# Kernel optimization log

Measured on AMD Instinct MI355X. Metric: run time of the kernel, lower is better.

The kernel has to match this reference:

```python
import jax, jax.numpy as jnp
import numpy as np
from jax import lax

D_MODEL = 1024
EXPAND = 2
D_INNER = EXPAND * D_MODEL  # 2048
D_STATE = 16
D_CONV = 4
DT_RANK = -(-D_INNER // 16)  # ceil(d_inner/16) = 128
BATCH, SEQLEN = 2, 1024
LN_EPS = 1e-5


def setup_inputs() -> dict:
    key = jax.random.key(0)
    ks = jax.random.split(key, 8)
    s = lambda n: 1.0 / np.sqrt(n)
    x = jax.random.normal(ks[0], (BATCH, SEQLEN, D_MODEL), jnp.float32)
    ln_gamma = jnp.ones((D_MODEL,), jnp.float32)
    ln_beta = jnp.zeros((D_MODEL,), jnp.float32)
    in_proj_w = jax.random.normal(ks[1], (D_MODEL, 2 * D_INNER), jnp.float32) * s(D_MODEL)
    conv_w = jax.random.normal(ks[2], (D_INNER, D_CONV), jnp.float32) * s(D_CONV)
    conv_b = jnp.zeros((D_INNER,), jnp.float32)
    x_proj_w = jax.random.normal(ks[3], (D_INNER, DT_RANK + 2 * D_STATE), jnp.float32) * s(D_INNER)
    dt_proj_w = jax.random.uniform(ks[4], (DT_RANK, D_INNER), jnp.float32,
                                   -DT_RANK ** -0.5, DT_RANK ** -0.5)
    # dt bias init: inverse-softplus of dt ~ LogUniform(1e-3, 1e-1)
    dt = jnp.exp(jax.random.uniform(ks[5], (D_INNER,), jnp.float32)
                 * (np.log(0.1) - np.log(0.001)) + np.log(0.001))
    dt = jnp.clip(dt, 1e-4)
    dt_proj_b = dt + jnp.log(-jnp.expm1(-dt))
    A_log = jnp.log(jnp.tile(jnp.arange(1, D_STATE + 1, dtype=jnp.float32)[None, :],
                             (D_INNER, 1)))  # (D_INNER, D_STATE)
    D_param = jnp.ones((D_INNER,), jnp.float32)
    out_proj_w = jax.random.normal(ks[6], (D_INNER, D_MODEL), jnp.float32) * s(D_INNER)
    return {"x": x, "ln_gamma": ln_gamma, "ln_beta": ln_beta, "in_proj_w": in_proj_w,
            "conv_w": conv_w, "conv_b": conv_b, "x_proj_w": x_proj_w,
            "dt_proj_w": dt_proj_w, "dt_proj_b": dt_proj_b, "A_log": A_log,
            "D_param": D_param, "out_proj_w": out_proj_w}


def _layernorm(x, gamma, beta):
    mu = jnp.mean(x, -1, keepdims=True)
    var = jnp.mean(jnp.square(x - mu), -1, keepdims=True)
    return (x - mu) * lax.rsqrt(var + LN_EPS) * gamma + beta


def reference(x, ln_gamma, ln_beta, in_proj_w, conv_w, conv_b, x_proj_w,
              dt_proj_w, dt_proj_b, A_log, D_param, out_proj_w):
    B, L, _ = x.shape
    residual = x
    h = _layernorm(x, ln_gamma, ln_beta)
    xz = h @ in_proj_w                               # (B, L, 2*Di)
    xb, z = jnp.split(xz, 2, axis=-1)                # each (B, L, Di)

    # Depthwise causal conv1d (left pad d_conv-1, truncate to L)
    xp = jnp.pad(xb, ((0, 0), (D_CONV - 1, 0), (0, 0)))
    xc = sum(xp[:, k:k + L, :] * conv_w[:, k] for k in range(D_CONV)) + conv_b
    xb = jax.nn.silu(xc)                             # (B, L, Di)

    # Selective SSM
    xpj = xb @ x_proj_w                              # (B, L, dt_rank + 2N)
    dt_r = xpj[..., :DT_RANK]
    B_mat = xpj[..., DT_RANK:DT_RANK + D_STATE]      # (B, L, N)
    C_mat = xpj[..., DT_RANK + D_STATE:]             # (B, L, N)
    delta = jax.nn.softplus(dt_r @ dt_proj_w + dt_proj_b)  # (B, L, Di)
    A = -jnp.exp(A_log)                              # (Di, N)
    dA = jnp.exp(delta[..., None] * A)               # (B, L, Di, N)
    dBx = delta[..., None] * B_mat[:, :, None, :] * xb[..., None]  # (B, L, Di, N)

    def step(hcar, inp):
        dA_t, dBx_t, C_t = inp                       # (B,Di,N),(B,Di,N),(B,N)
        hcar = dA_t * hcar + dBx_t
        y_t = jnp.einsum('bdn,bn->bd', hcar, C_t)
        return hcar, y_t

    h0 = jnp.zeros((B, D_INNER, D_STATE), xb.dtype)
    _, ys = lax.scan(step, h0, (dA.transpose(1, 0, 2, 3),
                                dBx.transpose(1, 0, 2, 3),
                                C_mat.transpose(1, 0, 2)))
    y = ys.transpose(1, 0, 2) + xb * D_param         # (B, L, Di)

    y = y * jax.nn.silu(z)
    return y @ out_proj_w + residual
```

## Files before the change

kernel.cpp:

```cpp
#include <hip/hip_runtime.h>
#include <hip/hip_bf16.h>

#define D_MODEL 1024
#define D_INNER 2048
#define NPROJ   4096
#define D_STATE 16
#define DT_RANK 128
#define XPJ_N   160
#define SEQLEN  1024
#define BATCH   2
#define NTOK    2048
#define CHUNK   32
#define NCHUNK  (SEQLEN / CHUNK)
#define LOG2_NCHUNK 5
#define SPLITK  8
#define OP_SPLITK 4

typedef short short8 __attribute__((ext_vector_type(8)));
typedef float f32x4 __attribute__((ext_vector_type(4)));

__device__ __forceinline__ float sigmoidf_(float x) { return 1.f / (1.f + __expf(-x)); }
__device__ __forceinline__ ushort f2bf_bits(float f) {
    __hip_bfloat16 h = __float2bfloat16(f);
    return *(ushort*)&h;
}
__device__ __forceinline__ float bf2f(ushort u) {
    union { unsigned int i; float f; } v;
    v.i = ((unsigned int)u) << 16;
    return v.f;
}
__device__ __forceinline__ float quad_xor1_add(float p) {
    int q = __builtin_amdgcn_mov_dpp(__float_as_int(p), 0xB1, 0xF, 0xF, true);
    return p + __int_as_float(q);
}
__device__ __forceinline__ float quad_xor2_add(float p) {
    int q = __builtin_amdgcn_mov_dpp(__float_as_int(p), 0x4E, 0xF, 0xF, true);
    return p + __int_as_float(q);
}

__global__ __launch_bounds__(256) void ln_kernel(const float* __restrict__ x,
                                                 const float* __restrict__ g,
                                                 const float* __restrict__ be,
                                                 ushort* __restrict__ hb)
{
    int row = blockIdx.x;
    const float4* xr = (const float4*)(x + (long)row * D_MODEL);
    float4 v = xr[threadIdx.x];
    float s1 = v.x + v.y + v.z + v.w;
    float s2 = v.x*v.x + v.y*v.y + v.z*v.z + v.w*v.w;
    for (int off = 32; off >= 1; off >>= 1) {
        s1 += __shfl_down(s1, off);
        s2 += __shfl_down(s2, off);
    }
    __shared__ float red[8];
    int wid = threadIdx.x >> 6;
    if ((threadIdx.x & 63) == 0) { red[wid] = s1; red[4 + wid] = s2; }
    __syncthreads();
    float mu  = (red[0] + red[1] + red[2] + red[3]) * (1.f / D_MODEL);
    float ex2 = (red[4] + red[5] + red[6] + red[7]) * (1.f / D_MODEL);
    float inv = rsqrtf(ex2 - mu * mu + 1e-5f);
    float4 g4 = ((const float4*)g)[threadIdx.x];
    float4 b4 = ((const float4*)be)[threadIdx.x];
    ushort4 o;
    o.x = f2bf_bits((v.x - mu) * inv * g4.x + b4.x);
    o.y = f2bf_bits((v.y - mu) * inv * g4.y + b4.y);
    o.z = f2bf_bits((v.z - mu) * inv * g4.z + b4.z);
    o.w = f2bf_bits((v.w - mu) * inv * g4.w + b4.w);
    *(ushort4*)(hb + (long)row * D_MODEL + threadIdx.x * 4) = o;
}

__global__ __launch_bounds__(256) void transpose_bf16_kernel(const float* __restrict__ in,
                                                             ushort* __restrict__ out,
                                                             int R, int C)
{
    __shared__ float tile[64][65];
    int c0 = blockIdx.x * 64, r0 = blockIdx.y * 64;
    #pragma unroll
    for (int i = 0; i < 16; ++i) {
        int idx = threadIdx.x + i * 256;
        int r = idx >> 6, c = idx & 63;
        tile[r][c] = (r0 + r < R && c0 + c < C) ? in[(long)(r0 + r) * C + (c0 + c)] : 0.f;
    }
    __syncthreads();
    #pragma unroll
    for (int i = 0; i < 16; ++i) {
        int idx = threadIdx.x + i * 256;
        int cc = idx >> 6, rr = idx & 63;
        if (c0 + cc < C && r0 + rr < R)
            out[(long)(c0 + cc) * R + (r0 + rr)] = f2bf_bits(tile[rr][cc]);
    }
}

template <int EPI, int OBF>
__global__ __launch_bounds__(256) void gemm_mfma_kernel(const ushort* __restrict__ A,
                                                        const ushort* __restrict__ Bt,
                                                        const float* __restrict__ bias,
                                                        float* __restrict__ Cf,
                                                        ushort* __restrict__ Cb,
                                                        int M, int N, int K, int lda, int ldb)
{
    long zoff = (long)blockIdx.z;
    A  += zoff * K;
    Bt += zoff * K;
    if (OBF == 0) Cf += zoff * (long)M * N;
    __shared__ __align__(16) ushort Al[128 * 32];
    __shared__ __align__(16) ushort Bl[128 * 32];
    int tid = threadIdx.x;
    int lane = tid & 63;
    int w = tid >> 6, wr = w >> 1, wc = w & 1;
    int m0 = blockIdx.y * 128, n0 = blockIdx.x * 128;
    f32x4 acc[4][4];
    #pragma unroll
    for (int m = 0; m < 4; ++m)
        #pragma unroll
        for (int n = 0; n < 4; ++n) acc[m][n] = (f32x4){0.f, 0.f, 0.f, 0.f};
    int l15 = lane & 15, kq = lane >> 4;

    for (int k0 = 0; k0 < K; k0 += 32) {
        #pragma unroll
        for (int i = 0; i < 2; ++i) {
            int s = i * 256 + tid;
            int row = s >> 2, kg = s & 3;
            int kgl = kg ^ ((row >> 1) & 3);
            __builtin_amdgcn_global_load_lds(
                (const __attribute__((address_space(1))) void*)(A + (long)(m0 + row) * lda + k0 + kgl * 8),
                (__attribute__((address_space(3))) void*)(Al + s * 8), 16, 0, 0);
            __builtin_amdgcn_global_load_lds(
                (const __attribute__((address_space(1))) void*)(Bt + (long)(n0 + row) * ldb + k0 + kgl * 8),
                (__attribute__((address_space(3))) void*)(Bl + s * 8), 16, 0, 0);
        }
        __syncthreads();
        short8 af[4], bf[4];
        #pragma unroll
        for (int m = 0; m < 4; ++m) {
            int row = wr * 64 + m * 16 + l15;
            af[m] = *(const short8*)&Al[row * 32 + (kq ^ ((row >> 1) & 3)) * 8];
        }
        #pragma unroll
        for (int n = 0; n < 4; ++n) {
            int row = wc * 64 + n * 16 + l15;
            bf[n] = *(const short8*)&Bl[row * 32 + (kq ^ ((row >> 1) & 3)) * 8];
        }
        #pragma unroll
        for (int m = 0; m < 4; ++m)
            #pragma unroll
            for (int n = 0; n < 4; ++n)
                acc[m][n] = __builtin_amdgcn_mfma_f32_16x16x32_bf16(af[m], bf[n], acc[m][n], 0, 0, 0);
        __syncthreads();
    }
    #pragma unroll
    for (int m = 0; m < 4; ++m) {
        #pragma unroll
        for (int n = 0; n < 4; ++n) {
            #pragma unroll
            for (int r = 0; r < 4; ++r) {
                int row = m0 + wr * 64 + m * 16 + kq * 4 + r;
                int col = n0 + wc * 64 + n * 16 + l15;
                float v = acc[m][n][r];
                if (EPI == 1) {
                    v += bias[col];
                    v = (v > 20.f) ? v : log1pf(__expf(v));
                }
                if (OBF) Cb[(long)row * N + col] = f2bf_bits(v);
                else     Cf[(long)row * N + col] = v;
            }
        }
    }
}

template <int EPI, int OBF>
__global__ __launch_bounds__(256) void gemm_mfma64_kernel(const ushort* __restrict__ A,
                                                          const ushort* __restrict__ Bt,
                                                          const float* __restrict__ bias,
                                                          float* __restrict__ Cf,
                                                          ushort* __restrict__ Cb,
                                                          int M, int N, int K)
{
    __shared__ __align__(16) ushort Al[128 * 32];
    __shared__ __align__(16) ushort Bl[64 * 32];
    int tid = threadIdx.x;
    int lane = tid & 63;
    int w = tid >> 6, wr = w >> 1, wc = w & 1;
    int m0 = blockIdx.y * 128, n0 = blockIdx.x * 64;
    f32x4 acc[4][2];
    #pragma unroll
    for (int m = 0; m < 4; ++m)
        #pragma unroll
        for (int n = 0; n < 2; ++n) acc[m][n] = (f32x4){0.f, 0.f, 0.f, 0.f};
    int l15 = lane & 15, kq = lane >> 4;

    for (int k0 = 0; k0 < K; k0 += 32) {
        #pragma unroll
        for (int i = 0; i < 2; ++i) {
            int s = i * 256 + tid;
            int row = s >> 2, kg = s & 3;
            int kgl = kg ^ ((row >> 1) & 3);
            __builtin_amdgcn_global_load_lds(
                (const __attribute__((address_space(1))) void*)(A + (long)(m0 + row) * K + k0 + kgl * 8),
                (__attribute__((address_space(3))) void*)(Al + s * 8), 16, 0, 0);
        }
        {
            int s = tid;
            int row = s >> 2, kg = s & 3;
            int kgl = kg ^ ((row >> 1) & 3);
            __builtin_amdgcn_global_load_lds(
                (const __attribute__((address_space(1))) void*)(Bt + (long)(n0 + row) * K + k0 + kgl * 8),
                (__attribute__((address_space(3))) void*)(Bl + s * 8), 16, 0, 0);
        }
        __syncthreads();
        short8 af[4], bf[2];
        #pragma unroll
        for (int m = 0; m < 4; ++m) {
            int row = wr * 64 + m * 16 + l15;
            af[m] = *(const short8*)&Al[row * 32 + (kq ^ ((row >> 1) & 3)) * 8];
        }
        #pragma unroll
        for (int n = 0; n < 2; ++n) {
            int row = wc * 32 + n * 16 + l15;
            bf[n] = *(const short8*)&Bl[row * 32 + (kq ^ ((row >> 1) & 3)) * 8];
        }
        #pragma unroll
        for (int m = 0; m < 4; ++m)
            #pragma unroll
            for (int n = 0; n < 2; ++n)
                acc[m][n] = __builtin_amdgcn_mfma_f32_16x16x32_bf16(af[m], bf[n], acc[m][n], 0, 0, 0);
        __syncthreads();
    }
    #pragma unroll
    for (int m = 0; m < 4; ++m) {
        #pragma unroll
        for (int n = 0; n < 2; ++n) {
            #pragma unroll
            for (int r = 0; r < 4; ++r) {
                int row = m0 + wr * 64 + m * 16 + kq * 4 + r;
                int col = n0 + wc * 32 + n * 16 + l15;
                float v = acc[m][n][r];
                if (EPI == 1) {
                    v += bias[col];
                    v = (v > 20.f) ? v : log1pf(__expf(v));
                }
                if (OBF) Cb[(long)row * N + col] = f2bf_bits(v);
                else     Cf[(long)row * N + col] = v;
            }
        }
    }
}

__global__ __launch_bounds__(256) void reduce_out_kernel(const float* __restrict__ Ppart,
                                                         const float* __restrict__ resid,
                                                         float* __restrict__ out)
{
    long i = (long)blockIdx.x * 256 + threadIdx.x;
    const long STRIDE = (long)NTOK * D_MODEL / 4;
    float4 s = ((const float4*)Ppart)[i];
    #pragma unroll
    for (int k = 1; k < OP_SPLITK; ++k) {
        float4 p = ((const float4*)Ppart)[k * STRIDE + i];
        s.x += p.x; s.y += p.y; s.z += p.z; s.w += p.w;
    }
    float4 r = ((const float4*)resid)[i];
    s.x += r.x; s.y += r.y; s.z += r.z; s.w += r.w;
    ((float4*)out)[i] = s;
}

__global__ __launch_bounds__(256) void gemm4_mfma_kernel(const ushort* __restrict__ A,
                                                         const ushort* __restrict__ Bt,
                                                         float* __restrict__ Ppart,
                                                         int M, int K)
{
    __shared__ __align__(16) ushort Al[64 * 32];
    __shared__ __align__(16) ushort Bl[160 * 32];
    int tid = threadIdx.x;
    int lane = tid & 63;
    int w = tid >> 6, wr = w >> 1, wc = w & 1;
    int sk = blockIdx.x;
    int m0 = blockIdx.y * 64;
    int kbase = sk * (K / SPLITK);
    f32x4 acc[2][5];
    #pragma unroll
    for (int m = 0; m < 2; ++m)
        #pragma unroll
        for (int n = 0; n < 5; ++n) acc[m][n] = (f32x4){0.f, 0.f, 0.f, 0.f};
    int l15 = lane & 15, kq = lane >> 4;

    for (int ks = 0; ks < K / SPLITK; ks += 32) {
        int k0 = kbase + ks;
        {
            int s = tid;
            int row = s >> 2, kg = s & 3;
            int kgl = kg ^ ((row >> 1) & 3);
            __builtin_amdgcn_global_load_lds(
                (const __attribute__((address_space(1))) void*)(A + (long)(m0 + row) * K + k0 + kgl * 8),
                (__attribute__((address_space(3))) void*)(Al + s * 8), 16, 0, 0);
        }
        #pragma unroll
        for (int i = 0; i < 3; ++i) {
            int s = i * 256 + tid;
            if (s < 640) {
                int row = s >> 2, kg = s & 3;
                int kgl = kg ^ ((row >> 1) & 3);
                __builtin_amdgcn_global_load_lds(
                    (const __attribute__((address_space(1))) void*)(Bt + (long)row * K + k0 + kgl * 8),
                    (__attribute__((address_space(3))) void*)(Bl + s * 8), 16, 0, 0);
            }
        }
        __syncthreads();
        short8 af[2], bf[5];
        #pragma unroll
        for (int m = 0; m < 2; ++m) {
            int row = wr * 32 + m * 16 + l15;
            af[m] = *(const short8*)&Al[row * 32 + (kq ^ ((row >> 1) & 3)) * 8];
        }
        #pragma unroll
        for (int n = 0; n < 5; ++n) {
            int row = wc * 80 + n * 16 + l15;
            bf[n] = *(const short8*)&Bl[row * 32 + (kq ^ ((row >> 1) & 3)) * 8];
        }
        #pragma unroll
        for (int m = 0; m < 2; ++m)
            #pragma unroll
            for (int n = 0; n < 5; ++n)
                acc[m][n] = __builtin_amdgcn_mfma_f32_16x16x32_bf16(af[m], bf[n], acc[m][n], 0, 0, 0);
        __syncthreads();
    }
    float* P = Ppart + (long)sk * M * XPJ_N;
    #pragma unroll
    for (int m = 0; m < 2; ++m) {
        #pragma unroll
        for (int n = 0; n < 5; ++n) {
            #pragma unroll
            for (int r = 0; r < 4; ++r) {
                int row = m0 + wr * 32 + m * 16 + kq * 4 + r;
                int col = wc * 80 + n * 16 + l15;
                P[(long)row * XPJ_N + col] = acc[m][n][r];
            }
        }
    }
}

__global__ __launch_bounds__(256) void reduce_xpj_kernel(const float* __restrict__ Ppart,
                                                         float* __restrict__ xpj,
                                                         ushort* __restrict__ dtr)
{
    long i = (long)blockIdx.x * 256 + threadIdx.x;
    float s = 0.f;
    #pragma unroll
    for (int k = 0; k < SPLITK; ++k) s += Ppart[k * (long)NTOK * XPJ_N + i];
    xpj[i] = s;
    int col = (int)(i % XPJ_N);
    long row = i / XPJ_N;
    if (col < DT_RANK) dtr[row * DT_RANK + col] = f2bf_bits(s);
}

__global__ __launch_bounds__(256) void conv_silu_kernel(const ushort* __restrict__ xzb,
                                                        const float* __restrict__ cw,
                                                        const float* __restrict__ cb,
                                                        ushort* __restrict__ xbb)
{
    long i = (long)blockIdx.x * 256 + threadIdx.x;
    int d = (int)(i & (D_INNER - 1));
    long tok = i >> 11;
    int l = (int)(tok & (SEQLEN - 1));
    float w0 = cw[d * 4 + 0], w1 = cw[d * 4 + 1], w2 = cw[d * 4 + 2], w3 = cw[d * 4 + 3];
    float acc = cb[d];
    acc += bf2f(xzb[tok * NPROJ + d]) * w3;
    if (l >= 1) acc += bf2f(xzb[(tok - 1) * NPROJ + d]) * w2;
    if (l >= 2) acc += bf2f(xzb[(tok - 2) * NPROJ + d]) * w1;
    if (l >= 3) acc += bf2f(xzb[(tok - 3) * NPROJ + d]) * w0;
    float v = acc * sigmoidf_(acc);
    xbb[i] = f2bf_bits(v);
}

__global__ __launch_bounds__(256) void scan_partial_kernel(const ushort* __restrict__ deltab,
                                                           const ushort* __restrict__ xbb,
                                                           const float* __restrict__ xpj,
                                                           const float* __restrict__ A_log,
                                                           float* __restrict__ Pout,
                                                           float* __restrict__ Hout)
{
    int tid = threadIdx.x;
    int j = tid & 3, grp = tid >> 2;
    long gidx = (long)blockIdx.x * 64 + grp;
    int d = (int)(gidx & (D_INNER - 1));
    int c = (int)((gidx >> 11) & (NCHUNK - 1));
    int b = (int)(gidx >> (11 + LOG2_NCHUNK));
    float4 al = *(const float4*)&A_log[d * D_STATE + 4 * j];
    float a0 = -__expf(al.x), a1 = -__expf(al.y), a2 = -__expf(al.z), a3 = -__expf(al.w);
    float h0 = 0.f, h1 = 0.f, h2 = 0.f, h3 = 0.f, cum = 0.f;
    long tok0 = (long)b * SEQLEN + c * CHUNK;
    const ushort* dp = deltab + tok0 * D_INNER + d;
    const ushort* xp = xbb + tok0 * D_INNER + d;
    const float* Bp = xpj + tok0 * XPJ_N + DT_RANK + 4 * j;
    for (int t = 0; t < CHUNK; ++t) {
        float dl = bf2f(*dp);
        float x  = bf2f(*xp);
        float4 Bv = *(const float4*)Bp;
        dp += D_INNER; xp += D_INNER; Bp += XPJ_N;
        cum += dl;
        float ux = dl * x;
        h0 = __expf(dl * a0) * h0 + ux * Bv.x;
        h1 = __expf(dl * a1) * h1 + ux * Bv.y;
        h2 = __expf(dl * a2) * h2 + ux * Bv.z;
        h3 = __expf(dl * a3) * h3 + ux * Bv.w;
    }
    long o = gidx * D_STATE + 4 * j;
    *(float4*)&Pout[o] = (float4){__expf(a0 * cum), __expf(a1 * cum), __expf(a2 * cum), __expf(a3 * cum)};
    *(float4*)&Hout[o] = (float4){h0, h1, h2, h3};
}

__global__ __launch_bounds__(256) void scan_chunkscan_kernel(const float* __restrict__ P,
                                                             const float* __restrict__ H,
                                                             float* __restrict__ hinit)
{
    long i = (long)blockIdx.x * 256 + threadIdx.x;
    int n = (int)(i & (D_STATE - 1));
    int d = (int)((i >> 4) & (D_INNER - 1));
    int b = (int)(i >> 15);
    float h = 0.f;
    for (int c = 0; c < NCHUNK; ++c) {
        long o = ((((long)b * NCHUNK + c) * D_INNER + d) * D_STATE) + n;
        hinit[o] = h;
        h = P[o] * h + H[o];
    }
}

__global__ __launch_bounds__(256) void scan_final_kernel(const ushort* __restrict__ deltab,
                                                         const ushort* __restrict__ xbb,
                                                         const float* __restrict__ xpj,
                                                         const ushort* __restrict__ xzb,
                                                         const float* __restrict__ A_log,
                                                         const float* __restrict__ Dp,
                                                         const float* __restrict__ hinit,
                                                         ushort* __restrict__ yb)
{
    int tid = threadIdx.x;
    int j = tid & 3, grp = tid >> 2;
    long gidx = (long)blockIdx.x * 64 + grp;
    int d = (int)(gidx & (D_INNER - 1));
    int c = (int)((gidx >> 11) & (NCHUNK - 1));
    int b = (int)(gidx >> (11 + LOG2_NCHUNK));
    float4 al = *(const float4*)&A_log[d * D_STATE + 4 * j];
    float a0 = -__expf(al.x), a1 = -__expf(al.y), a2 = -__expf(al.z), a3 = -__expf(al.w);
    float dpar = Dp[d];
    float4 hv = *(const float4*)&hinit[gidx * D_STATE + 4 * j];
    float h0 = hv.x, h1 = hv.y, h2 = hv.z, h3 = hv.w;
    long tok0 = (long)b * SEQLEN + c * CHUNK;
    const ushort* dp = deltab + tok0 * D_INNER + d;
    const ushort* xp = xbb + tok0 * D_INNER + d;
    const float* Bp = xpj + tok0 * XPJ_N + DT_RANK + 4 * j;
    const float* Cp = Bp + D_STATE;
    const ushort* zp = xzb + tok0 * NPROJ + D_INNER + d;
    ushort* yp = yb + tok0 * D_INNER + d;
    for (int t = 0; t < CHUNK; ++t) {
        float dl = bf2f(*dp);
        float x  = bf2f(*xp);
        float4 Bv = *(const float4*)Bp;
        float4 Cv = *(const float4*)Cp;
        dp += D_INNER; xp += D_INNER; Bp += XPJ_N; Cp += XPJ_N;
        float ux = dl * x;
        h0 = __expf(dl * a0) * h0 + ux * Bv.x;
        h1 = __expf(dl * a1) * h1 + ux * Bv.y;
        h2 = __expf(dl * a2) * h2 + ux * Bv.z;
        h3 = __expf(dl * a3) * h3 + ux * Bv.w;
        float p = h0 * Cv.x + h1 * Cv.y + h2 * Cv.z + h3 * Cv.w;
        p = quad_xor1_add(p);
        p = quad_xor2_add(p);
        if (j == 0) {
            float z = bf2f(*zp);
            float y = p + x * dpar;
            *yp = f2bf_bits(y * (z * sigmoidf_(z)));
        }
        zp += NPROJ; yp += D_INNER;
    }
}

extern "C" void kernel_launch(void* const* d_in, const int* in_sizes, int n_in,
                              void* d_out, int out_size, void* d_ws, size_t ws_size,
                              hipStream_t stream) {
    const float* x         = (const float*)d_in[0];
    const float* ln_gamma  = (const float*)d_in[1];
    const float* ln_beta   = (const float*)d_in[2];
    const float* in_proj_w = (const float*)d_in[3];
    const float* conv_w    = (const float*)d_in[4];
    const float* conv_b    = (const float*)d_in[5];
    const float* x_proj_w  = (const float*)d_in[6];
    const float* dt_proj_w = (const float*)d_in[7];
    const float* dt_proj_b = (const float*)d_in[8];
    const float* A_log     = (const float*)d_in[9];
    const float* D_param   = (const float*)d_in[10];
    const float* out_proj_w= (const float*)d_in[11];
    float* out = (float*)d_out;

    float* p = (float*)d_ws;
    ushort* hb      = (ushort*)p; p += 1048576;
    ushort* W2T     = (ushort*)p; p += 2097152;
    ushort* W7T     = (ushort*)p; p += 1048576;
    ushort* XPT     = (ushort*)p; p += 163840;
    ushort* DTT     = (ushort*)p; p += 131072;
    ushort* xz_bf16 = (ushort*)p; p += 4194304;
    ushort* xb_bf16 = (ushort*)p; p += 2097152;
    float*  xpj     = p;          p += 327680;
    ushort* dtr     = (ushort*)p; p += 131072;
    ushort* delta_bf16 = (ushort*)p; p += 2097152;
    float*  Ppart   = p;          p += 2621440;
    float*  Pbuf    = p;          p += 2097152;
    float*  Hbuf    = p;          p += 2097152;
    float*  hinit   = p;          p += 2097152;
    ushort* y_bf16  = (ushort*)p; p += 2097152;
    float*  PpartO  = p;          p += 8388608;

    transpose_bf16_kernel<<<dim3(NPROJ / 64, D_MODEL / 64), 256, 0, stream>>>(
        in_proj_w, W2T, D_MODEL, NPROJ);
    transpose_bf16_kernel<<<dim3(D_MODEL / 64, D_INNER / 64), 256, 0, stream>>>(
        out_proj_w, W7T, D_INNER, D_MODEL);
    transpose_bf16_kernel<<<dim3((XPJ_N + 63) / 64, D_INNER / 64), 256, 0, stream>>>(
        x_proj_w, XPT, D_INNER, XPJ_N);
    transpose_bf16_kernel<<<dim3(D_INNER / 64, DT_RANK / 64), 256, 0, stream>>>(
        dt_proj_w, DTT, DT_RANK, D_INNER);

    ln_kernel<<<NTOK, 256, 0, stream>>>(x, ln_gamma, ln_beta, hb);

    gemm_mfma_kernel<0, 1><<<dim3(NPROJ / 128, NTOK / 128), 256, 0, stream>>>(
        hb, W2T, nullptr, nullptr, xz_bf16, NTOK, NPROJ, D_MODEL, D_MODEL, D_MODEL);

    conv_silu_kernel<<<(NTOK * D_INNER) / 256, 256, 0, stream>>>(
        xz_bf16, conv_w, conv_b, xb_bf16);

    gemm4_mfma_kernel<<<dim3(SPLITK, NTOK / 64), 256, 0, stream>>>(
        xb_bf16, XPT, Ppart, NTOK, D_INNER);
    reduce_xpj_kernel<<<(NTOK * XPJ_N) / 256, 256, 0, stream>>>(Ppart, xpj, dtr);

    gemm_mfma64_kernel<1, 1><<<dim3(D_INNER / 64, NTOK / 128), 256, 0, stream>>>(
        dtr, DTT, dt_proj_b, nullptr, delta_bf16, NTOK, D_INNER, DT_RANK);

    scan_partial_kernel<<<(BATCH * NCHUNK * D_INNER) / 64, 256, 0, stream>>>(
        delta_bf16, xb_bf16, xpj, A_log, Pbuf, Hbuf);
    scan_chunkscan_kernel<<<(BATCH * D_INNER * D_STATE) / 256, 256, 0, stream>>>(
        Pbuf, Hbuf, hinit);
    scan_final_kernel<<<(BATCH * NCHUNK * D_INNER) / 64, 256, 0, stream>>>(
        delta_bf16, xb_bf16, xpj, xz_bf16, A_log, D_param, hinit, y_bf16);

    gemm_mfma_kernel<0, 0><<<dim3(D_MODEL / 128, NTOK / 128, OP_SPLITK), 256, 0, stream>>>(
        y_bf16, W7T, nullptr, PpartO, nullptr, NTOK, D_MODEL, D_INNER / OP_SPLITK,
        D_INNER, D_INNER);
    reduce_out_kernel<<<(NTOK * D_MODEL / 4) / 256, 256, 0, stream>>>(PpartO, x, out);
}
```

Before: 203.4 us.

## Map one thread per channel with all 16 states in the scan kernels

Both chunked-scan kernels now give each thread one inner channel holding all 16 state values in registers, instead of spreading the states over four lanes. This removes the DPP cross-lane reduction, the single-lane output write and the replicated delta/x/z loads per quad, and makes the bf16 loads coalesced across channels. The exp calls switch to exp2f with A prescaled by log2(e). In exchange the grid drops from 2048 to 512 blocks, so each thread carries more registers and there is less parallelism to hide latency.

```diff
diff --git a/kernel.cpp b/kernel.cpp
--- a/kernel.cpp
+++ b/kernel.cpp
@@ -29,14 +29,7 @@
     v.i = ((unsigned int)u) << 16;
     return v.f;
 }
-__device__ __forceinline__ float quad_xor1_add(float p) {
-    int q = __builtin_amdgcn_mov_dpp(__float_as_int(p), 0xB1, 0xF, 0xF, true);
-    return p + __int_as_float(q);
-}
-__device__ __forceinline__ float quad_xor2_add(float p) {
-    int q = __builtin_amdgcn_mov_dpp(__float_as_int(p), 0x4E, 0xF, 0xF, true);
-    return p + __int_as_float(q);
-}
+#define LOG2E 1.44269504088896f
 
 __global__ __launch_bounds__(256) void ln_kernel(const float* __restrict__ x,
                                                  const float* __restrict__ g,
@@ -371,6 +364,7 @@
     xbb[i] = f2bf_bits(v);
 }
 
+
 __global__ __launch_bounds__(256) void scan_partial_kernel(const ushort* __restrict__ deltab,
                                                            const ushort* __restrict__ xbb,
                                                            const float* __restrict__ xpj,
@@ -378,34 +372,51 @@
                                                            float* __restrict__ Pout,
                                                            float* __restrict__ Hout)
 {
-    int tid = threadIdx.x;
-    int j = tid & 3, grp = tid >> 2;
-    long gidx = (long)blockIdx.x * 64 + grp;
-    int d = (int)(gidx & (D_INNER - 1));
-    int c = (int)((gidx >> 11) & (NCHUNK - 1));
-    int b = (int)(gidx >> (11 + LOG2_NCHUNK));
-    float4 al = *(const float4*)&A_log[d * D_STATE + 4 * j];
-    float a0 = -__expf(al.x), a1 = -__expf(al.y), a2 = -__expf(al.z), a3 = -__expf(al.w);
-    float h0 = 0.f, h1 = 0.f, h2 = 0.f, h3 = 0.f, cum = 0.f;
+    int blk = blockIdx.x;
+    int db = blk & 7;
+    int c  = (blk >> 3) & (NCHUNK - 1);
+    int b  = blk >> (3 + LOG2_NCHUNK);
+    int d  = db * 256 + threadIdx.x;
+    float a[16], h[16];
+    #pragma unroll
+    for (int q = 0; q < 4; ++q) {
+        float4 al = *(const float4*)&A_log[d * D_STATE + q * 4];
+        a[q*4+0] = -__expf(al.x) * LOG2E;
+        a[q*4+1] = -__expf(al.y) * LOG2E;
+        a[q*4+2] = -__expf(al.z) * LOG2E;
+        a[q*4+3] = -__expf(al.w) * LOG2E;
+    }
+    #pragma unroll
+    for (int n = 0; n < 16; ++n) h[n] = 0.f;
+    float cum = 0.f;
     long tok0 = (long)b * SEQLEN + c * CHUNK;
     const ushort* dp = deltab + tok0 * D_INNER + d;
     const ushort* xp = xbb + tok0 * D_INNER + d;
-    const float* Bp = xpj + tok0 * XPJ_N + DT_RANK + 4 * j;
+    const float* Bbase = xpj + tok0 * XPJ_N + DT_RANK;
     for (int t = 0; t < CHUNK; ++t) {
-        float dl = bf2f(*dp);
-        float x  = bf2f(*xp);
-        float4 Bv = *(const float4*)Bp;
-        dp += D_INNER; xp += D_INNER; Bp += XPJ_N;
+        float dl = bf2f(dp[(long)t * D_INNER]);
+        float x  = bf2f(xp[(long)t * D_INNER]);
+        float ux = dl * x;
         cum += dl;
-        float ux = dl * x;
-        h0 = __expf(dl * a0) * h0 + ux * Bv.x;
-        h1 = __expf(dl * a1) * h1 + ux * Bv.y;
-        h2 = __expf(dl * a2) * h2 + ux * Bv.z;
-        h3 = __expf(dl * a3) * h3 + ux * Bv.w;
-    }
-    long o = gidx * D_STATE + 4 * j;
-    *(float4*)&Pout[o] = (float4){__expf(a0 * cum), __expf(a1 * cum), __expf(a2 * cum), __expf(a3 * cum)};
-    *(float4*)&Hout[o] = (float4){h0, h1, h2, h3};
+        const float* Bp = Bbase + (long)t * XPJ_N;
+        #pragma unroll
+        for (int q = 0; q < 4; ++q) {
+            float4 Bv = *(const float4*)(Bp + q * 4);
+            h[q*4+0] = exp2f(dl * a[q*4+0]) * h[q*4+0] + ux * Bv.x;
+            h[q*4+1] = exp2f(dl * a[q*4+1]) * h[q*4+1] + ux * Bv.y;
+            h[q*4+2] = exp2f(dl * a[q*4+2]) * h[q*4+2] + ux * Bv.z;
+            h[q*4+3] = exp2f(dl * a[q*4+3]) * h[q*4+3] + ux * Bv.w;
+        }
+    }
+    long chbase = ((long)(b * NCHUNK + c) * D_INNER + d) * D_STATE;
+    #pragma unroll
+    for (int q = 0; q < 4; ++q) {
+        float4 pv = {exp2f(a[q*4+0] * cum), exp2f(a[q*4+1] * cum),
+                     exp2f(a[q*4+2] * cum), exp2f(a[q*4+3] * cum)};
+        *(float4*)&Pout[chbase + q * 4] = pv;
+        float4 hv = {h[q*4+0], h[q*4+1], h[q*4+2], h[q*4+3]};
+        *(float4*)&Hout[chbase + q * 4] = hv;
+    }
 }
 
 __global__ __launch_bounds__(256) void scan_chunkscan_kernel(const float* __restrict__ P,
@@ -433,44 +444,52 @@
                                                          const float* __restrict__ hinit,
                                                          ushort* __restrict__ yb)
 {
-    int tid = threadIdx.x;
-    int j = tid & 3, grp = tid >> 2;
-    long gidx = (long)blockIdx.x * 64 + grp;
-    int d = (int)(gidx & (D_INNER - 1));
-    int c = (int)((gidx >> 11) & (NCHUNK - 1));
-    int b = (int)(gidx >> (11 + LOG2_NCHUNK));
-    float4 al = *(const float4*)&A_log[d * D_STATE + 4 * j];
-    float a0 = -__expf(al.x), a1 = -__expf(al.y), a2 = -__expf(al.z), a3 = -__expf(al.w);
+    int blk = blockIdx.x;
+    int db = blk & 7;
+    int c  = (blk >> 3) & (NCHUNK - 1);
+    int b  = blk >> (3 + LOG2_NCHUNK);
+    int d  = db * 256 + threadIdx.x;
+    float a[16], h[16];
+    #pragma unroll
+    for (int q = 0; q < 4; ++q) {
+        float4 al = *(const float4*)&A_log[d * D_STATE + q * 4];
+        a[q*4+0] = -__expf(al.x) * LOG2E;
+        a[q*4+1] = -__expf(al.y) * LOG2E;
+        a[q*4+2] = -__expf(al.z) * LOG2E;
+        a[q*4+3] = -__expf(al.w) * LOG2E;
+    }
+    long chbase = ((long)(b * NCHUNK + c) * D_INNER + d) * D_STATE;
+    #pragma unroll
+    for (int q = 0; q < 4; ++q) {
+        float4 hv = *(const float4*)&hinit[chbase + q * 4];
+        h[q*4+0] = hv.x; h[q*4+1] = hv.y; h[q*4+2] = hv.z; h[q*4+3] = hv.w;
+    }
     float dpar = Dp[d];
-    float4 hv = *(const float4*)&hinit[gidx * D_STATE + 4 * j];
-    float h0 = hv.x, h1 = hv.y, h2 = hv.z, h3 = hv.w;
     long tok0 = (long)b * SEQLEN + c * CHUNK;
     const ushort* dp = deltab + tok0 * D_INNER + d;
     const ushort* xp = xbb + tok0 * D_INNER + d;
-    const float* Bp = xpj + tok0 * XPJ_N + DT_RANK + 4 * j;
-    const float* Cp = Bp + D_STATE;
     const ushort* zp = xzb + tok0 * NPROJ + D_INNER + d;
     ushort* yp = yb + tok0 * D_INNER + d;
+    const float* Bbase = xpj + tok0 * XPJ_N + DT_RANK;
     for (int t = 0; t < CHUNK; ++t) {
-        float dl = bf2f(*dp);
-        float x  = bf2f(*xp);
-        float4 Bv = *(const float4*)Bp;
-        float4 Cv = *(const float4*)Cp;
-        dp += D_INNER; xp += D_INNER; Bp += XPJ_N; Cp += XPJ_N;
+        float dl = bf2f(dp[(long)t * D_INNER]);
+        float x  = bf2f(xp[(long)t * D_INNER]);
+        float z  = bf2f(zp[(long)t * NPROJ]);
         float ux = dl * x;
-        h0 = __expf(dl * a0) * h0 + ux * Bv.x;
-        h1 = __expf(dl * a1) * h1 + ux * Bv.y;
-        h2 = __expf(dl * a2) * h2 + ux * Bv.z;
-        h3 = __expf(dl * a3) * h3 + ux * Bv.w;
-        float p = h0 * Cv.x + h1 * Cv.y + h2 * Cv.z + h3 * Cv.w;
-        p = quad_xor1_add(p);
-        p = quad_xor2_add(p);
-        if (j == 0) {
-            float z = bf2f(*zp);
-            float y = p + x * dpar;
-            *yp = f2bf_bits(y * (z * sigmoidf_(z)));
-        }
-        zp += NPROJ; yp += D_INNER;
+        const float* Bp = Bbase + (long)t * XPJ_N;
+        float y = 0.f;
+        #pragma unroll
+        for (int q = 0; q < 4; ++q) {
+            float4 Bv = *(const float4*)(Bp + q * 4);
+            float4 Cv = *(const float4*)(Bp + D_STATE + q * 4);
+            h[q*4+0] = exp2f(dl * a[q*4+0]) * h[q*4+0] + ux * Bv.x;
+            h[q*4+1] = exp2f(dl * a[q*4+1]) * h[q*4+1] + ux * Bv.y;
+            h[q*4+2] = exp2f(dl * a[q*4+2]) * h[q*4+2] + ux * Bv.z;
+            h[q*4+3] = exp2f(dl * a[q*4+3]) * h[q*4+3] + ux * Bv.w;
+            y += h[q*4+0] * Cv.x + h[q*4+1] * Cv.y + h[q*4+2] * Cv.z + h[q*4+3] * Cv.w;
+        }
+        y += x * dpar;
+        yp[(long)t * D_INNER] = f2bf_bits(y * (z * sigmoidf_(z)));
     }
 }
 
@@ -533,11 +552,11 @@
     gemm_mfma64_kernel<1, 1><<<dim3(D_INNER / 64, NTOK / 128), 256, 0, stream>>>(
         dtr, DTT, dt_proj_b, nullptr, delta_bf16, NTOK, D_INNER, DT_RANK);
 
-    scan_partial_kernel<<<(BATCH * NCHUNK * D_INNER) / 64, 256, 0, stream>>>(
+    scan_partial_kernel<<<BATCH * NCHUNK * 8, 256, 0, stream>>>(
         delta_bf16, xb_bf16, xpj, A_log, Pbuf, Hbuf);
     scan_chunkscan_kernel<<<(BATCH * D_INNER * D_STATE) / 256, 256, 0, stream>>>(
         Pbuf, Hbuf, hinit);
-    scan_final_kernel<<<(BATCH * NCHUNK * D_INNER) / 64, 256, 0, stream>>>(
+    scan_final_kernel<<<BATCH * NCHUNK * 8, 256, 0, stream>>>(
         delta_bf16, xb_bf16, xpj, xz_bf16, A_log, D_param, hinit, y_bf16);
 
     gemm_mfma_kernel<0, 0><<<dim3(D_MODEL / 128, NTOK / 128, OP_SPLITK), 256, 0, stream>>>(
```

Result: slower. 208.6 us (+2.6%).
